# Optimization experiments

Hardware: AMD Instinct MI355X
Metric: run time of the kernel (lower is better)

Reference implementation:

```python
import jax, jax.numpy as jnp
import numpy as np

N_NODES = 10000
N_EDGES = 640000
IN_CH = 128
HID_CH = 128


def setup_inputs() -> dict:
    key = jax.random.key(0)
    ks = jax.random.split(key, 6)
    x = jax.random.normal(ks[0], (N_NODES, IN_CH), dtype=jnp.float32)
    edge_index = jax.random.randint(ks[1], (2, N_EDGES), 0, N_NODES, dtype=jnp.int32)
    # GCNConv weights (glorot-ish scale) and biases
    W1 = jax.random.normal(ks[2], (IN_CH, HID_CH), dtype=jnp.float32) / np.float32(np.sqrt(IN_CH))
    b1 = jnp.zeros((HID_CH,), jnp.float32)
    W2 = jax.random.normal(ks[3], (HID_CH, HID_CH), dtype=jnp.float32) / np.float32(np.sqrt(HID_CH))
    b2 = jnp.zeros((HID_CH,), jnp.float32)
    prelu_a = jnp.full((HID_CH,), 0.25, jnp.float32)  # nn.PReLU(hidden) init
    return {"x": x, "edge_index": edge_index, "W1": W1, "b1": b1,
            "W2": W2, "b2": b2, "prelu_a": prelu_a}


def _gcn_conv(x, W, b, src, dst, norm, n_nodes):
    # x: [N, Fin] -> transform, gather by src, scale by sym-norm, scatter-add to dst
    h = x @ W                                   # [N, Fout]
    msg = h[src] * norm[:, None]                # [E+N, Fout] gather (irregular)
    out = jax.ops.segment_sum(msg, dst, num_segments=n_nodes)
    return out + b


def reference(x, edge_index, W1, b1, W2, b2, prelu_a):
    n = x.shape[0]
    # PyG GCNConv default: add self-loops, symmetric D^{-1/2} A D^{-1/2} norm
    loops = jnp.arange(n, dtype=edge_index.dtype)
    src = jnp.concatenate([edge_index[0], loops])
    dst = jnp.concatenate([edge_index[1], loops])
    deg = jax.ops.segment_sum(jnp.ones_like(dst, dtype=jnp.float32), dst,
                              num_segments=n)
    dinv = jax.lax.rsqrt(jnp.maximum(deg, 1.0))  # deg >= 1 due to self-loops
    norm = dinv[src] * dinv[dst]                 # [E+N]

    h = _gcn_conv(x, W1, b1, src, dst, norm, n)
    h = jnp.where(h > 0, h, prelu_a * h)         # per-channel PReLU
    # Dropout(p=0.1) is identity in eval mode (correctness baseline)
    out = _gcn_conv(h, W2, b2, src, dst, norm, n)
    return out
```

## Files before the change

### kernel.cpp

```cpp
#include <hip/hip_runtime.h>

#define CH 128
#define SLOT_CAP 128
#define BSHIFT 6
#define BNODES 64
#define MAXB 256
#define CAPB 4608
#define CSTRIDE 32
#define EPB 2048

typedef float    fvec4 __attribute__((ext_vector_type(4)));
typedef unsigned uvec4 __attribute__((ext_vector_type(4)));
typedef unsigned uvec2 __attribute__((ext_vector_type(2)));

__device__ __forceinline__ unsigned short f2bf(float f) {
    union { float f; unsigned int u; } v; v.f = f;
    unsigned int u = v.u;
    u += 0x7FFFu + ((u >> 16) & 1u);
    return (unsigned short)(u >> 16);
}
__device__ __forceinline__ float bflo(unsigned int p) {
    union { unsigned int u; float f; } v; v.u = p << 16; return v.f;
}
__device__ __forceinline__ float bfhi(unsigned int p) {
    union { unsigned int u; float f; } v; v.u = p & 0xFFFF0000u; return v.f;
}

__global__ __launch_bounds__(256) void part_kernel(const int* __restrict__ src,
                                                   const int* __restrict__ dst,
                                                   int* __restrict__ bcur,
                                                   unsigned* __restrict__ bbuf,
                                                   int E, int nb) {
    __shared__ int cnt[MAXB];
    __shared__ int base[MAXB];
    int t = threadIdx.x;
    for (int i = t; i < nb; i += 256) cnt[i] = 0;
    __syncthreads();
    int e0 = blockIdx.x * EPB;
    unsigned pkt[8];
    int rk[8];
#pragma unroll
    for (int i = 0; i < 8; ++i) {
        int e = e0 + i * 256 + t;
        pkt[i] = 0xFFFFFFFFu;
        rk[i] = -1;
        if (e < E) {
            int d = __builtin_nontemporal_load(dst + e);
            int s = __builtin_nontemporal_load(src + e);
            pkt[i] = (unsigned)d | ((unsigned)s << 16);
            rk[i] = atomicAdd(&cnt[d >> BSHIFT], 1);
        }
    }
    __syncthreads();
    for (int b = t; b < nb; b += 256) {
        int c = cnt[b];
        base[b] = c ? atomicAdd(&bcur[(size_t)b * CSTRIDE], c) : 0;
    }
    __syncthreads();
#pragma unroll
    for (int i = 0; i < 8; ++i) {
        if (rk[i] < 0) continue;
        int b = (pkt[i] & 0xFFFFu) >> BSHIFT;
        int idx = base[b] + rk[i];
        if (idx < CAPB) bbuf[(size_t)b * CAPB + idx] = pkt[i];
    }
}

__global__ __launch_bounds__(256) void build_kernel(const unsigned* __restrict__ bbuf,
                                                    const int* __restrict__ bcur,
                                                    unsigned short* __restrict__ slots,
                                                    int* __restrict__ deg,
                                                    int N) {
    __shared__ int lcnt[BNODES];
    int b = blockIdx.x, t = threadIdx.x;
    if (t < BNODES) lcnt[t] = 0;
    __syncthreads();
    int cnt = bcur[(size_t)b * CSTRIDE];
    if (cnt > CAPB) cnt = CAPB;
    const unsigned* bp = bbuf + (size_t)b * CAPB;
    for (int i = t; i < cnt; i += 256) {
        unsigned pkt = bp[i];
        int d = pkt & 0xFFFFu;
        int r = atomicAdd(&lcnt[d - (b << BSHIFT)], 1);
        if (r < SLOT_CAP)
            slots[((size_t)d << 7) + r] = (unsigned short)(pkt >> 16);
    }
    __syncthreads();
    if (t < BNODES) {
        int node = (b << BSHIFT) + t;
        if (node < N) deg[node] = lcnt[t];
    }
}

__global__ __launch_bounds__(256, 5) void gemmp_kernel(const float* __restrict__ A,
                                                       const float* __restrict__ W,
                                                       const int* __restrict__ deg,
                                                       unsigned short* __restrict__ Cb,
                                                       int M) {
    __shared__ float Ws[128 * 64];
    int t = threadIdx.x;
    int tile = blockIdx.x >> 1;
    int c0 = (blockIdx.x & 1) * 64;
    fvec4* Ws4 = (fvec4*)Ws;
    const fvec4* Wg = (const fvec4*)W;
#pragma unroll
    for (int i = 0; i < 8; ++i) {
        int idx = t + i * 256;
        int k = idx >> 4, c = idx & 15;
        Ws4[idx] = Wg[k * 32 + (c0 >> 2) + c];
    }
    __syncthreads();
    int rg = t >> 4, cg = t & 15;
    int row0 = tile * 32 + rg * 2;
    bool v0 = row0 < M, v1 = row0 + 1 < M;
    const fvec4* Ar0 = (const fvec4*)(A + (size_t)(v0 ? row0 : 0) * CH);
    const fvec4* Ar1 = (const fvec4*)(A + (size_t)(v1 ? row0 + 1 : 0) * CH);
    fvec4 acc0 = {0.f,0.f,0.f,0.f}, acc1 = {0.f,0.f,0.f,0.f};
#pragma unroll 4
    for (int k4 = 0; k4 < 32; ++k4) {
        fvec4 a0 = Ar0[k4], a1 = Ar1[k4];
#pragma unroll
        for (int j = 0; j < 4; ++j) {
            fvec4 w = Ws4[(k4 * 4 + j) * 16 + cg];
            acc0 += a0[j] * w;
            acc1 += a1[j] * w;
        }
    }
#pragma unroll
    for (int r = 0; r < 2; ++r) {
        bool v = r ? v1 : v0;
        if (!v) continue;
        int rr = row0 + r;
        fvec4 s = r ? acc1 : acc0;
        float dn = rsqrtf((float)(deg[rr] + 1));
        ((ushort4*)(Cb + (size_t)rr * CH + c0))[cg] =
            make_ushort4(f2bf(dn * s.x), f2bf(dn * s.y),
                         f2bf(dn * s.z), f2bf(dn * s.w));
    }
}

__global__ __launch_bounds__(256) void agg_kernel(const unsigned short* __restrict__ hb,
                                                  const unsigned short* __restrict__ slots,
                                                  const int* __restrict__ deg,
                                                  const float* __restrict__ bias,
                                                  const float* __restrict__ prelu_a,
                                                  float* __restrict__ outp,
                                                  int N, int apply_prelu) {
    int wave = threadIdx.x >> 6, lane = threadIdx.x & 63;
    int node = blockIdx.x * 4 + wave;
    if (node >= N) return;
    int dg = deg[node];
    if (dg > SLOT_CAP) dg = SLOT_CAP;
    int half = lane >> 5, sl = lane & 31;
    const uvec4* sp4 = (const uvec4*)(slots + ((size_t)node << 7));
    const unsigned short* hbl = hb + 4 * sl;
    uvec2 sv = *(const uvec2*)(hbl + ((size_t)node << 7));
    float a0 = 0.f, a1 = 0.f, a2 = 0.f, a3 = 0.f;
    int nbatch = dg >> 4, rem = dg & 15;
    uvec4 qa, qb, qan, qbn;
    if (dg > 0) { qa = sp4[0]; qb = sp4[1]; }
    for (int b = 0; b < nbatch; ++b) {
        bool more = (b + 1 < nbatch) || (rem != 0);
        if (more) { qan = sp4[2 * b + 2]; qbn = sp4[2 * b + 3]; }
        unsigned q[8] = {qa.x, qa.y, qa.z, qa.w, qb.x, qb.y, qb.z, qb.w};
        uvec2 p[8];
#pragma unroll
        for (int j = 0; j < 8; ++j) {
            unsigned idx = half ? (q[j] >> 16) : (q[j] & 0xFFFFu);
            p[j] = *(const uvec2*)(hbl + (size_t)idx * CH);
        }
#pragma unroll
        for (int j = 0; j < 8; ++j) {
            a0 += bflo(p[j].x); a1 += bfhi(p[j].x);
            a2 += bflo(p[j].y); a3 += bfhi(p[j].y);
        }
        qa = qan; qb = qbn;
    }
    if (rem) {
        int k = nbatch << 4;
        unsigned q[8] = {qa.x, qa.y, qa.z, qa.w, qb.x, qb.y, qb.z, qb.w};
#pragma unroll
        for (int j = 0; j < 8; ++j) {
            unsigned raw = half ? (q[j] >> 16) : (q[j] & 0xFFFFu);
            unsigned idx = raw < (unsigned)N ? raw : 0u;
            uvec2 pv = *(const uvec2*)(hbl + (size_t)idx * CH);
            if (k + 2 * j + half < dg) {
                a0 += bflo(pv.x); a1 += bfhi(pv.x);
                a2 += bflo(pv.y); a3 += bfhi(pv.y);
            }
        }
    }
    a0 += __shfl_xor(a0, 32);
    a1 += __shfl_xor(a1, 32);
    a2 += __shfl_xor(a2, 32);
    a3 += __shfl_xor(a3, 32);
    if (half == 0) {
        a0 += bflo(sv.x); a1 += bfhi(sv.x);
        a2 += bflo(sv.y); a3 += bfhi(sv.y);
        float dn = rsqrtf((float)(dg + 1));
        fvec4 bv = ((const fvec4*)bias)[sl];
        float r0 = dn * a0 + bv.x;
        float r1 = dn * a1 + bv.y;
        float r2 = dn * a2 + bv.z;
        float r3 = dn * a3 + bv.w;
        if (apply_prelu) {
            fvec4 av = ((const fvec4*)prelu_a)[sl];
            r0 = r0 > 0.f ? r0 : av.x * r0;
            r1 = r1 > 0.f ? r1 : av.y * r1;
            r2 = r2 > 0.f ? r2 : av.z * r2;
            r3 = r3 > 0.f ? r3 : av.w * r3;
        }
        fvec4 rv = {r0, r1, r2, r3};
        ((fvec4*)(outp + (size_t)node * CH))[sl] = rv;
    }
}


extern "C" void kernel_launch(void* const* d_in, const int* in_sizes, int n_in,
                              void* d_out, int out_size, void* d_ws, size_t ws_size,
                              hipStream_t stream) {
    const float* x  = (const float*)d_in[0];
    const int*   ei = (const int*)d_in[1];
    const float* W1 = (const float*)d_in[2];
    const float* b1 = (const float*)d_in[3];
    const float* W2 = (const float*)d_in[4];
    const float* b2 = (const float*)d_in[5];
    const float* pa = (const float*)d_in[6];

    int N = in_sizes[0] / CH;
    int E = in_sizes[1] / 2;
    const int* src = ei;
    const int* dst = ei + E;
    int nb = (N + BNODES - 1) >> BSHIFT;

    char* w = (char*)d_ws;
    auto alloc = [&](size_t bytes) {
        void* p = (void*)w;
        w += (bytes + 255) & ~(size_t)255;
        return p;
    };
    int*            bcur   = (int*)alloc((size_t)nb * CSTRIDE * 4);
    unsigned*       bbuf   = (unsigned*)alloc((size_t)nb * CAPB * 4);
    unsigned short* slots  = (unsigned short*)alloc((size_t)N * SLOT_CAP * 2);
    int*            deg    = (int*)alloc((size_t)N * 4);
    unsigned short* bufAb  = (unsigned short*)alloc((size_t)N * CH * 2);
    float*          bufB   = (float*)alloc((size_t)N * CH * 4);
    float*          outp   = (float*)d_out;

    int ntiles = (N + 31) / 32;
    int npb = (E + EPB - 1) / EPB;

    hipMemsetAsync(bcur, 0, (size_t)nb * CSTRIDE * 4, stream);

    part_kernel<<<npb, 256, 0, stream>>>(src, dst, bcur, bbuf, E, nb);
    build_kernel<<<nb, 256, 0, stream>>>(bbuf, bcur, slots, deg, N);

    gemmp_kernel<<<2 * ntiles, 256, 0, stream>>>(x, W1, deg, bufAb, N);
    agg_kernel<<<(N + 3) / 4, 256, 0, stream>>>(bufAb, slots, deg, b1, pa, bufB, N, 1);

    gemmp_kernel<<<2 * ntiles, 256, 0, stream>>>(bufB, W2, deg, bufAb, N);
    agg_kernel<<<(N + 3) / 4, 256, 0, stream>>>(bufAb, slots, deg, b2, pa, outp, N, 0);
}
```

Before: 144.7 us.

## Replace global bucket atomics with per-block partitions and software-pipeline gather loads

The partition step now writes each block's per-bucket counts and packets into fixed slots of capacity PCAP, so the global atomics and the memset are no longer needed. The build kernel now uses one wave per partition chunk, at 512 threads per block. The aggregation kernel now prefetches the next batch's gathered feature rows, not just their indices, so gather latency overlaps with accumulation. This costs more registers, and any bucket chunk holding more than 64 edges silently drops the extras (with ~2048 edges spread over 157 buckets, the mean is about 13 per chunk).

```diff
diff --git a/kernel.cpp b/kernel.cpp
--- a/kernel.cpp
+++ b/kernel.cpp
@@ -5,8 +5,7 @@
 #define BSHIFT 6
 #define BNODES 64
 #define MAXB 256
-#define CAPB 4608
-#define CSTRIDE 32
+#define PCAP 64
 #define EPB 2048
 
 typedef float    fvec4 __attribute__((ext_vector_type(4)));
@@ -28,15 +27,14 @@
 
 __global__ __launch_bounds__(256) void part_kernel(const int* __restrict__ src,
                                                    const int* __restrict__ dst,
-                                                   int* __restrict__ bcur,
+                                                   int* __restrict__ gcnt,
                                                    unsigned* __restrict__ bbuf,
-                                                   int E, int nb) {
+                                                   int E, int nb, int npb) {
     __shared__ int cnt[MAXB];
-    __shared__ int base[MAXB];
-    int t = threadIdx.x;
+    int t = threadIdx.x, blk = blockIdx.x;
     for (int i = t; i < nb; i += 256) cnt[i] = 0;
     __syncthreads();
-    int e0 = blockIdx.x * EPB;
+    int e0 = blk * EPB;
     unsigned pkt[8];
     int rk[8];
 #pragma unroll
@@ -52,38 +50,36 @@
         }
     }
     __syncthreads();
-    for (int b = t; b < nb; b += 256) {
-        int c = cnt[b];
-        base[b] = c ? atomicAdd(&bcur[(size_t)b * CSTRIDE], c) : 0;
-    }
-    __syncthreads();
+    for (int b = t; b < nb; b += 256)
+        gcnt[(size_t)b * npb + blk] = cnt[b];
 #pragma unroll
     for (int i = 0; i < 8; ++i) {
-        if (rk[i] < 0) continue;
+        if (rk[i] < 0 || rk[i] >= PCAP) continue;
         int b = (pkt[i] & 0xFFFFu) >> BSHIFT;
-        int idx = base[b] + rk[i];
-        if (idx < CAPB) bbuf[(size_t)b * CAPB + idx] = pkt[i];
-    }
-}
-
-__global__ __launch_bounds__(256) void build_kernel(const unsigned* __restrict__ bbuf,
-                                                    const int* __restrict__ bcur,
+        bbuf[((size_t)b * npb + blk) * PCAP + rk[i]] = pkt[i];
+    }
+}
+
+__global__ __launch_bounds__(512) void build_kernel(const unsigned* __restrict__ bbuf,
+                                                    const int* __restrict__ gcnt,
                                                     unsigned short* __restrict__ slots,
                                                     int* __restrict__ deg,
-                                                    int N) {
+                                                    int N, int npb) {
     __shared__ int lcnt[BNODES];
     int b = blockIdx.x, t = threadIdx.x;
     if (t < BNODES) lcnt[t] = 0;
     __syncthreads();
-    int cnt = bcur[(size_t)b * CSTRIDE];
-    if (cnt > CAPB) cnt = CAPB;
-    const unsigned* bp = bbuf + (size_t)b * CAPB;
-    for (int i = t; i < cnt; i += 256) {
-        unsigned pkt = bp[i];
-        int d = pkt & 0xFFFFu;
-        int r = atomicAdd(&lcnt[d - (b << BSHIFT)], 1);
-        if (r < SLOT_CAP)
-            slots[((size_t)d << 7) + r] = (unsigned short)(pkt >> 16);
+    int wv = t >> 6, lane = t & 63;
+    for (int j = wv; j < npb; j += 8) {
+        int cj = gcnt[(size_t)b * npb + j];
+        if (cj > PCAP) cj = PCAP;
+        unsigned pkt = bbuf[((size_t)b * npb + j) * PCAP + lane];
+        if (lane < cj) {
+            int d = pkt & 0xFFFFu;
+            int r = atomicAdd(&lcnt[d - (b << BSHIFT)], 1);
+            if (r < SLOT_CAP)
+                slots[((size_t)d << 7) + r] = (unsigned short)(pkt >> 16);
+        }
     }
     __syncthreads();
     if (t < BNODES) {
@@ -156,37 +152,42 @@
     const unsigned short* hbl = hb + 4 * sl;
     uvec2 sv = *(const uvec2*)(hbl + ((size_t)node << 7));
     float a0 = 0.f, a1 = 0.f, a2 = 0.f, a3 = 0.f;
-    int nbatch = dg >> 4, rem = dg & 15;
-    uvec4 qa, qb, qan, qbn;
-    if (dg > 0) { qa = sp4[0]; qb = sp4[1]; }
-    for (int b = 0; b < nbatch; ++b) {
-        bool more = (b + 1 < nbatch) || (rem != 0);
-        if (more) { qan = sp4[2 * b + 2]; qbn = sp4[2 * b + 3]; }
+    int nfull = dg >> 4, rem = dg & 15, nbt = (dg + 15) >> 4;
+    uvec2 pc[8], pn[8];
+    if (nbt > 0) {
+        uvec4 qa = sp4[0], qb = sp4[1];
         unsigned q[8] = {qa.x, qa.y, qa.z, qa.w, qb.x, qb.y, qb.z, qb.w};
-        uvec2 p[8];
 #pragma unroll
         for (int j = 0; j < 8; ++j) {
             unsigned idx = half ? (q[j] >> 16) : (q[j] & 0xFFFFu);
-            p[j] = *(const uvec2*)(hbl + (size_t)idx * CH);
+            pc[j] = *(const uvec2*)(hbl + (size_t)idx * CH);
+        }
+    }
+    for (int b = 0; b < nfull; ++b) {
+        if (b + 1 < nbt) {
+            uvec4 qa = sp4[2 * b + 2], qb = sp4[2 * b + 3];
+            unsigned q[8] = {qa.x, qa.y, qa.z, qa.w, qb.x, qb.y, qb.z, qb.w};
+#pragma unroll
+            for (int j = 0; j < 8; ++j) {
+                unsigned idx = half ? (q[j] >> 16) : (q[j] & 0xFFFFu);
+                pn[j] = *(const uvec2*)(hbl + (size_t)idx * CH);
+            }
         }
 #pragma unroll
         for (int j = 0; j < 8; ++j) {
-            a0 += bflo(p[j].x); a1 += bfhi(p[j].x);
-            a2 += bflo(p[j].y); a3 += bfhi(p[j].y);
-        }
-        qa = qan; qb = qbn;
+            a0 += bflo(pc[j].x); a1 += bfhi(pc[j].x);
+            a2 += bflo(pc[j].y); a3 += bfhi(pc[j].y);
+        }
+#pragma unroll
+        for (int j = 0; j < 8; ++j) pc[j] = pn[j];
     }
     if (rem) {
-        int k = nbatch << 4;
-        unsigned q[8] = {qa.x, qa.y, qa.z, qa.w, qb.x, qb.y, qb.z, qb.w};
+        int k = nfull << 4;
 #pragma unroll
         for (int j = 0; j < 8; ++j) {
-            unsigned raw = half ? (q[j] >> 16) : (q[j] & 0xFFFFu);
-            unsigned idx = raw < (unsigned)N ? raw : 0u;
-            uvec2 pv = *(const uvec2*)(hbl + (size_t)idx * CH);
             if (k + 2 * j + half < dg) {
-                a0 += bflo(pv.x); a1 += bfhi(pv.x);
-                a2 += bflo(pv.y); a3 += bfhi(pv.y);
+                a0 += bflo(pc[j].x); a1 += bfhi(pc[j].x);
+                a2 += bflo(pc[j].y); a3 += bfhi(pc[j].y);
             }
         }
     }
@@ -232,6 +233,7 @@
     const int* src = ei;
     const int* dst = ei + E;
     int nb = (N + BNODES - 1) >> BSHIFT;
+    int npb = (E + EPB - 1) / EPB;
 
     char* w = (char*)d_ws;
     auto alloc = [&](size_t bytes) {
@@ -239,8 +241,8 @@
         w += (bytes + 255) & ~(size_t)255;
         return p;
     };
-    int*            bcur   = (int*)alloc((size_t)nb * CSTRIDE * 4);
-    unsigned*       bbuf   = (unsigned*)alloc((size_t)nb * CAPB * 4);
+    int*            gcnt   = (int*)alloc((size_t)nb * npb * 4);
+    unsigned*       bbuf   = (unsigned*)alloc((size_t)nb * npb * PCAP * 4);
     unsigned short* slots  = (unsigned short*)alloc((size_t)N * SLOT_CAP * 2);
     int*            deg    = (int*)alloc((size_t)N * 4);
     unsigned short* bufAb  = (unsigned short*)alloc((size_t)N * CH * 2);
@@ -248,12 +250,9 @@
     float*          outp   = (float*)d_out;
 
     int ntiles = (N + 31) / 32;
-    int npb = (E + EPB - 1) / EPB;
-
-    hipMemsetAsync(bcur, 0, (size_t)nb * CSTRIDE * 4, stream);
-
-    part_kernel<<<npb, 256, 0, stream>>>(src, dst, bcur, bbuf, E, nb);
-    build_kernel<<<nb, 256, 0, stream>>>(bbuf, bcur, slots, deg, N);
+
+    part_kernel<<<npb, 256, 0, stream>>>(src, dst, gcnt, bbuf, E, nb, npb);
+    build_kernel<<<nb, 512, 0, stream>>>(bbuf, gcnt, slots, deg, N, npb);
 
     gemmp_kernel<<<2 * ntiles, 256, 0, stream>>>(x, W1, deg, bufAb, N);
     agg_kernel<<<(N + 3) / 4, 256, 0, stream>>>(bufAb, slots, deg, b1, pa, bufB, N, 1);
```

Result: slower. 156.9 us (+8.5%).

## Split aggregation channels across two blocks per node group

Applied to the files above, without the earlier changes.

The aggregation kernel now splits the 128 channels into two halves handled by separate blocks, interleaved in groups of four so that both halves of a node group are scheduled close together. Each lane gathers 4 bytes (2 bf16) instead of 8, doubling the block count and the parallelism available to hide gather latency. The cost is that slot indices and degrees are read twice, and each gather request is narrower, so more memory instructions are issued per byte fetched.

```diff
diff --git a/kernel.cpp b/kernel.cpp
--- a/kernel.cpp
+++ b/kernel.cpp
@@ -146,16 +146,19 @@
                                                   const float* __restrict__ prelu_a,
                                                   float* __restrict__ outp,
                                                   int N, int apply_prelu) {
+    int bid = blockIdx.x;
     int wave = threadIdx.x >> 6, lane = threadIdx.x & 63;
-    int node = blockIdx.x * 4 + wave;
+    int h = (bid >> 2) & 1;
+    int j = ((bid >> 3) << 2) | (bid & 3);
+    int node = j * 4 + wave;
     if (node >= N) return;
     int dg = deg[node];
     if (dg > SLOT_CAP) dg = SLOT_CAP;
-    int half = lane >> 5, sl = lane & 31;
+    int par = lane >> 5, sl = lane & 31;
     const uvec4* sp4 = (const uvec4*)(slots + ((size_t)node << 7));
-    const unsigned short* hbl = hb + 4 * sl;
-    uvec2 sv = *(const uvec2*)(hbl + ((size_t)node << 7));
-    float a0 = 0.f, a1 = 0.f, a2 = 0.f, a3 = 0.f;
+    const unsigned short* hbl = hb + 64 * h + 2 * sl;
+    unsigned sv = *(const unsigned*)(hbl + ((size_t)node << 7));
+    float a0 = 0.f, a1 = 0.f;
     int nbatch = dg >> 4, rem = dg & 15;
     uvec4 qa, qb, qan, qbn;
     if (dg > 0) { qa = sp4[0]; qb = sp4[1]; }
@@ -163,16 +166,16 @@
         bool more = (b + 1 < nbatch) || (rem != 0);
         if (more) { qan = sp4[2 * b + 2]; qbn = sp4[2 * b + 3]; }
         unsigned q[8] = {qa.x, qa.y, qa.z, qa.w, qb.x, qb.y, qb.z, qb.w};
-        uvec2 p[8];
-#pragma unroll
-        for (int j = 0; j < 8; ++j) {
-            unsigned idx = half ? (q[j] >> 16) : (q[j] & 0xFFFFu);
-            p[j] = *(const uvec2*)(hbl + (size_t)idx * CH);
-        }
-#pragma unroll
-        for (int j = 0; j < 8; ++j) {
-            a0 += bflo(p[j].x); a1 += bfhi(p[j].x);
-            a2 += bflo(p[j].y); a3 += bfhi(p[j].y);
+        unsigned p[8];
+#pragma unroll
+        for (int jj = 0; jj < 8; ++jj) {
+            unsigned idx = par ? (q[jj] >> 16) : (q[jj] & 0xFFFFu);
+            p[jj] = *(const unsigned*)(hbl + (size_t)idx * CH);
+        }
+#pragma unroll
+        for (int jj = 0; jj < 8; ++jj) {
+            a0 += bflo(p[jj]);
+            a1 += bfhi(p[jj]);
         }
         qa = qan; qb = qbn;
     }
@@ -180,38 +183,31 @@
         int k = nbatch << 4;
         unsigned q[8] = {qa.x, qa.y, qa.z, qa.w, qb.x, qb.y, qb.z, qb.w};
 #pragma unroll
-        for (int j = 0; j < 8; ++j) {
-            unsigned raw = half ? (q[j] >> 16) : (q[j] & 0xFFFFu);
+        for (int jj = 0; jj < 8; ++jj) {
+            unsigned raw = par ? (q[jj] >> 16) : (q[jj] & 0xFFFFu);
             unsigned idx = raw < (unsigned)N ? raw : 0u;
-            uvec2 pv = *(const uvec2*)(hbl + (size_t)idx * CH);
-            if (k + 2 * j + half < dg) {
-                a0 += bflo(pv.x); a1 += bfhi(pv.x);
-                a2 += bflo(pv.y); a3 += bfhi(pv.y);
+            unsigned pv = *(const unsigned*)(hbl + (size_t)idx * CH);
+            if (k + 2 * jj + par < dg) {
+                a0 += bflo(pv);
+                a1 += bfhi(pv);
             }
         }
     }
     a0 += __shfl_xor(a0, 32);
     a1 += __shfl_xor(a1, 32);
-    a2 += __shfl_xor(a2, 32);
-    a3 += __shfl_xor(a3, 32);
-    if (half == 0) {
-        a0 += bflo(sv.x); a1 += bfhi(sv.x);
-        a2 += bflo(sv.y); a3 += bfhi(sv.y);
+    if (par == 0) {
+        a0 += bflo(sv);
+        a1 += bfhi(sv);
         float dn = rsqrtf((float)(dg + 1));
-        fvec4 bv = ((const fvec4*)bias)[sl];
+        float2 bv = ((const float2*)(bias + 64 * h))[sl];
         float r0 = dn * a0 + bv.x;
         float r1 = dn * a1 + bv.y;
-        float r2 = dn * a2 + bv.z;
-        float r3 = dn * a3 + bv.w;
         if (apply_prelu) {
-            fvec4 av = ((const fvec4*)prelu_a)[sl];
+            float2 av = ((const float2*)(prelu_a + 64 * h))[sl];
             r0 = r0 > 0.f ? r0 : av.x * r0;
             r1 = r1 > 0.f ? r1 : av.y * r1;
-            r2 = r2 > 0.f ? r2 : av.z * r2;
-            r3 = r3 > 0.f ? r3 : av.w * r3;
-        }
-        fvec4 rv = {r0, r1, r2, r3};
-        ((fvec4*)(outp + (size_t)node * CH))[sl] = rv;
+        }
+        ((float2*)(outp + (size_t)node * CH + 64 * h))[sl] = make_float2(r0, r1);
     }
 }
 
@@ -249,6 +245,8 @@
 
     int ntiles = (N + 31) / 32;
     int npb = (E + EPB - 1) / EPB;
+    int J = (N + 3) / 4;
+    int aggblk = ((J + 3) >> 2) << 3;
 
     hipMemsetAsync(bcur, 0, (size_t)nb * CSTRIDE * 4, stream);
 
@@ -256,8 +254,8 @@
     build_kernel<<<nb, 256, 0, stream>>>(bbuf, bcur, slots, deg, N);
 
     gemmp_kernel<<<2 * ntiles, 256, 0, stream>>>(x, W1, deg, bufAb, N);
-    agg_kernel<<<(N + 3) / 4, 256, 0, stream>>>(bufAb, slots, deg, b1, pa, bufB, N, 1);
+    agg_kernel<<<aggblk, 256, 0, stream>>>(bufAb, slots, deg, b1, pa, bufB, N, 1);
 
     gemmp_kernel<<<2 * ntiles, 256, 0, stream>>>(bufB, W2, deg, bufAb, N);
-    agg_kernel<<<(N + 3) / 4, 256, 0, stream>>>(bufAb, slots, deg, b2, pa, outp, N, 0);
-}
+    agg_kernel<<<aggblk, 256, 0, stream>>>(bufAb, slots, deg, b2, pa, outp, N, 0);
+}
```

Result: no change. 146.9 us (+1.5%).
